# Kernel tuning notes

Hardware: AMD Instinct MI355X
Metric: run time of the kernel (lower is better)

The kernel has to match this reference:

```python
import jax, jax.numpy as jnp
import numpy as np

B, S, H = 2, 112, 768
M = 256     # cfg.mlp_hidden_size
L = 54      # vocab size of 'ent_rel_id' (joint labels)
O = 10      # ent_rel_file['q_num_logits']


def setup_inputs() -> dict:
    key = jax.random.key(0)
    ks = jax.random.split(key, 12)
    inp = {
        "seq_encoder_reprs": jax.random.normal(ks[0], (B, S, H), jnp.float32),
        "joint_label_matrix": jax.random.randint(ks[1], (B, S, S), 0, L),
        "joint_label_matrix_mask": jax.random.randint(ks[2], (B, S, S), 0, 2) > 0,
        "quintuplet_matrix": jax.random.randint(ks[3], (B, S, S, S), 0, O),
        "quintuplet_matrix_mask": jax.random.randint(ks[4], (B, S, S, S), 0, 2) > 0,
        # learned parameters (BertLinear = Linear + activation; dropout inactive at eval)
        "pair_w": jax.random.normal(ks[5], (2 * H, M), jnp.float32) * 0.02,
        "pair_b": jnp.zeros((M,), jnp.float32),
        "final_w": jax.random.normal(ks[6], (M, L), jnp.float32) * 0.02,
        "final_b": jnp.zeros((L,), jnp.float32),
        "value_w": jax.random.normal(ks[7], (H, M), jnp.float32) * 0.02,
        "value_b": jnp.zeros((M,), jnp.float32),
        # U is zero-initialized in the module; use small random values so the
        # triaffine path produces non-trivial numerics.
        "U": jax.random.normal(ks[8], (O, M, M), jnp.float32) * 0.02,
    }
    return inp


def _masked_ce(logits, labels, mask):
    # mean cross-entropy over masked positions (== CE over boolean-indexed rows)
    logp = jax.nn.log_softmax(logits, axis=-1)
    nll = -jnp.take_along_axis(logp, labels[..., None], axis=-1)[..., 0]
    m = mask.astype(logits.dtype)
    return jnp.sum(nll * m) / jnp.maximum(jnp.sum(m), 1.0)


def reference(seq_encoder_reprs, joint_label_matrix, joint_label_matrix_mask,
              quintuplet_matrix, quintuplet_matrix_mask,
              pair_w, pair_b, final_w, final_b, value_w, value_b, U):
    x = seq_encoder_reprs  # [B,S,H]
    # pair = cat(head_expand, tail_expand) -> pair_mlp (Linear + GELU)
    # split the Linear over the concat to avoid materializing [B,S,S,2H]:
    # cat([head,tail]) @ W == head @ W[:H] + tail @ W[H:]
    h_part = jnp.einsum('bxh,hm->bxm', x, pair_w[:H])   # head contribution
    t_part = jnp.einsum('byh,hm->bym', x, pair_w[H:])   # tail contribution
    pair = jax.nn.gelu(h_part[:, :, None, :] + t_part[:, None, :, :] + pair_b,
                       approximate=False)               # [B,S,S,M]
    joint_score = jnp.einsum('bxym,ml->bxyl', pair, final_w) + final_b  # [B,S,S,L]

    value = jax.nn.gelu(jnp.einsum('bzh,hm->bzm', x, value_w) + value_b,
                        approximate=False)              # [B,S,M]
    # triaffine: bxyi,oij,bzj->bxyzo ; contract value with U first (small interm.)
    vU = jnp.einsum('bzj,oij->bzoi', value, U)          # [B,S,O,M]
    q_score = jnp.einsum('bxyi,bzoi->bxyzo', pair, vU)  # [B,S,S,S,O]

    # q_loss: CrossEntropy applied to softmax(q_score) (as in the source)
    q_probs = jax.nn.softmax(q_score, axis=-1)
    q_loss = _masked_ce(q_probs, quintuplet_matrix, quintuplet_matrix_mask)
    element_loss = _masked_ce(joint_score, joint_label_matrix, joint_label_matrix_mask)
    loss = element_loss + q_loss
    return loss, joint_score, q_score
```

## Files before the change

### kernel.cpp

```cpp
#include <hip/hip_runtime.h>
#include <hip/hip_bf16.h>

#define BB 2
#define SS 112
#define HH 768
#define MM 256
#define LL 54
#define OO 10
#define NPAIR (BB*SS*SS)
#define NQPOS (BB*SS*SS*SS)
#define SO (SS*OO)
#define SOP 1152
#define S2 (SS*SS)
#define NQBLK (NQPOS/512)
#define NEBLK (NPAIR/256)

typedef short bf16x8 __attribute__((ext_vector_type(8)));
typedef float f32x4 __attribute__((ext_vector_type(4)));

#define WS_HP    64
#define WS_TP    57408
#define WS_VAL   114752
#define WS_UT    172096
#define WS_VUB   827456
#define WS_PAIRB 1122368
#define WS_FWB   4333632
#define WS_QPART 4341824
#define WS_EPART 4352800

__device__ __forceinline__ float gelu_exact(float v) {
    return 0.5f * v * (1.0f + erff(v * 0.70710678118654752f));
}

__global__ __launch_bounds__(256) void k_proj(const float* __restrict__ x,
                                              const float* __restrict__ pw,
                                              const float* __restrict__ vw,
                                              const float* __restrict__ vb,
                                              float* __restrict__ hp,
                                              float* __restrict__ tp,
                                              float* __restrict__ val) {
    __shared__ float xs[HH];
    const int row = blockIdx.x;
    const int sel = blockIdx.y;
    const float* xr = x + (long)row * HH;
    for (int i = threadIdx.x; i < HH; i += 256) xs[i] = xr[i];
    __syncthreads();
    const int m = threadIdx.x;
    const float* w = (sel == 0) ? pw : (sel == 1) ? (pw + (long)HH * MM) : vw;
    float a = 0.f;
    for (int h = 0; h < HH; ++h)
        a = fmaf(xs[h], w[(long)h * MM + m], a);
    if (sel == 0)      hp[(long)row * MM + m] = a;
    else if (sel == 1) tp[(long)row * MM + m] = a;
    else               val[(long)row * MM + m] = gelu_exact(a + vb[m]);
}

__global__ void k_transU(const float* __restrict__ U, float* __restrict__ UT) {
    __shared__ float t[32][33];
    const int o = blockIdx.z;
    const int i0 = blockIdx.x * 32, j0 = blockIdx.y * 32;
    const int tx = threadIdx.x, ty = threadIdx.y;
    for (int r = 0; r < 32; r += 8)
        t[ty + r][tx] = U[((long)(o * MM + i0 + ty + r)) * MM + j0 + tx];
    __syncthreads();
    for (int r = 0; r < 32; r += 8)
        UT[((long)(o * MM + j0 + ty + r)) * MM + i0 + tx] = t[tx][ty + r];
}

__global__ __launch_bounds__(256) void k_vU(const float* __restrict__ val,
                                            const float* __restrict__ UT,
                                            __hip_bfloat16* __restrict__ vub) {
    __shared__ float vs[8][MM];
    const int b = blockIdx.x / 14, zt = blockIdx.x % 14, o = blockIdx.y;
    const int z0 = zt * 8;
    for (int idx = threadIdx.x; idx < 8 * MM; idx += 256) {
        const int zz = idx >> 8, m = idx & 255;
        vs[zz][m] = val[((long)(b * SS + z0 + zz)) * MM + m];
    }
    __syncthreads();
    const int i = threadIdx.x;
    float acc[8];
#pragma unroll
    for (int zz = 0; zz < 8; ++zz) acc[zz] = 0.f;
    const float* utp = UT + (long)o * MM * MM + i;
    for (int j = 0; j < MM; ++j) {
        const float u = utp[(long)j * MM];
#pragma unroll
        for (int zz = 0; zz < 8; ++zz) acc[zz] = fmaf(vs[zz][j], u, acc[zz]);
    }
#pragma unroll
    for (int zz = 0; zz < 8; ++zz)
        vub[((long)b * SOP + (z0 + zz) * OO + o) * MM + i] = __float2bfloat16(acc[zz]);
}

__global__ __launch_bounds__(256) void k_prepB(const float* __restrict__ fw,
                                               __hip_bfloat16* __restrict__ fwb) {
    const int idx = blockIdx.x * 256 + threadIdx.x;
    const int c = idx >> 8, k = idx & 255;
    const float v = (c < LL) ? fw[(long)k * LL + c] : 0.f;
    fwb[idx] = __float2bfloat16(v);
}

__global__ __launch_bounds__(256) void k_pair(const float* __restrict__ hp,
                                              const float* __restrict__ tp,
                                              const float* __restrict__ pb,
                                              __hip_bfloat16* __restrict__ pairb) {
    __shared__ float hs[MM];
    const int bx = blockIdx.x;
    hs[threadIdx.x] = hp[(long)bx * MM + threadIdx.x] + pb[threadIdx.x];
    __syncthreads();
    const int b = bx / SS;
    const int half = threadIdx.x >> 7;
    const int m0 = (threadIdx.x & 127) * 2;
    const float h0 = hs[m0], h1 = hs[m0 + 1];
    const int y0base = blockIdx.y * 56;
    for (int y0 = y0base; y0 < y0base + 56; y0 += 2) {
        const int y = y0 + half;
        const float2 t2 = *(const float2*)(tp + ((long)(b * SS + y)) * MM + m0);
        __hip_bfloat162 o2;
        o2.x = __float2bfloat16(gelu_exact(h0 + t2.x));
        o2.y = __float2bfloat16(gelu_exact(h1 + t2.y));
        *(__hip_bfloat162*)(pairb + ((long)bx * SS + y) * MM + m0) = o2;
    }
}

__global__ __launch_bounds__(256) void k_jointg(const __hip_bfloat16* __restrict__ pairb,
                                                const __hip_bfloat16* __restrict__ fwb,
                                                const float* __restrict__ fb,
                                                float* __restrict__ joint) {
    __shared__ __align__(16) char Al[16384];
    __shared__ __align__(16) char Bl[8192];
    const int r0 = blockIdx.x * 128;
    const int tid = threadIdx.x;
    const int lane = tid & 63, wid = tid >> 6;
    const int rl = lane & 15, kb = lane >> 4;

    int arow[4], aci[4], wadA[4];
#pragma unroll
    for (int j = 0; j < 4; ++j) {
        const int chunk = tid + 256 * j;
        arow[j] = chunk >> 3; aci[j] = chunk & 7;
        wadA[j] = (arow[j] * 128 + aci[j] * 16) ^ ((arow[j] & 7) << 4);
    }
    int brow[2], bci[2], wadB[2];
#pragma unroll
    for (int j = 0; j < 2; ++j) {
        const int chunk = tid + 256 * j;
        brow[j] = chunk >> 3; bci[j] = chunk & 7;
        wadB[j] = (brow[j] * 128 + bci[j] * 16) ^ ((brow[j] & 7) << 4);
    }

    f32x4 acc[2][4] = {};
    float4 ra[4], rb[2];

    auto issue = [&](int kt) {
#pragma unroll
        for (int j = 0; j < 4; ++j)
            ra[j] = *(const float4*)((const char*)pairb +
                     ((long)(r0 + arow[j]) * MM + kt * 64 + aci[j] * 8) * 2);
#pragma unroll
        for (int j = 0; j < 2; ++j)
            rb[j] = *(const float4*)((const char*)fwb +
                     ((long)brow[j] * MM + kt * 64 + bci[j] * 8) * 2);
    };
    auto dowrite = [&]() {
#pragma unroll
        for (int j = 0; j < 4; ++j) *(float4*)(Al + wadA[j]) = ra[j];
#pragma unroll
        for (int j = 0; j < 2; ++j) *(float4*)(Bl + wadB[j]) = rb[j];
    };
    auto compute = [&]() {
#pragma unroll
        for (int ks = 0; ks < 2; ++ks) {
            bf16x8 af[2], bv[4];
#pragma unroll
            for (int m = 0; m < 2; ++m) {
                const int rr = wid * 32 + m * 16 + rl;
                af[m] = *(const bf16x8*)(Al + ((rr * 128 + ks * 64 + kb * 16) ^ ((rr & 7) << 4)));
            }
#pragma unroll
            for (int n = 0; n < 4; ++n) {
                const int cc = n * 16 + rl;
                bv[n] = *(const bf16x8*)(Bl + ((cc * 128 + ks * 64 + kb * 16) ^ ((cc & 7) << 4)));
            }
#pragma unroll
            for (int m = 0; m < 2; ++m)
#pragma unroll
                for (int n = 0; n < 4; ++n)
                    acc[m][n] = __builtin_amdgcn_mfma_f32_16x16x32_bf16(af[m], bv[n], acc[m][n], 0, 0, 0);
        }
    };

    issue(0); dowrite(); __syncthreads();
    for (int kt = 0; kt < 4; ++kt) {
        if (kt < 3) issue(kt + 1);
        compute();
        __syncthreads();
        if (kt < 3) { dowrite(); __syncthreads(); }
    }

#pragma unroll
    for (int m = 0; m < 2; ++m)
#pragma unroll
        for (int n = 0; n < 4; ++n) {
            const int col = n * 16 + rl;
            if (col < LL) {
                const float bias = fb[col];
                const int rbase = r0 + wid * 32 + m * 16 + kb * 4;
#pragma unroll
                for (int j = 0; j < 4; ++j)
                    joint[(long)(rbase + j) * LL + col] = acc[m][n][j] + bias;
            }
        }
}

__global__ __launch_bounds__(256) void k_qgemm(const __hip_bfloat16* __restrict__ pairb,
                                               const __hip_bfloat16* __restrict__ vub,
                                               float* __restrict__ qout) {
    __shared__ __align__(16) char Al[16384];
    __shared__ __align__(16) char Bl[16384];
    const int b = blockIdx.z;
    const int r0 = blockIdx.x * 128;
    const int c0 = blockIdx.y * 128;
    const __hip_bfloat16* A  = pairb + (long)b * S2 * MM;
    const __hip_bfloat16* Bm = vub + (long)b * SOP * MM;
    const int tid = threadIdx.x;
    const int lane = tid & 63, wid = tid >> 6;
    const int wr = wid >> 1, wc = wid & 1;
    const int rl = lane & 15, kb = lane >> 4;

    int arow[4], aci[4], wad[4];
#pragma unroll
    for (int j = 0; j < 4; ++j) {
        const int chunk = tid + 256 * j;
        arow[j] = chunk >> 3; aci[j] = chunk & 7;
        wad[j] = (arow[j] * 128 + aci[j] * 16) ^ ((arow[j] & 7) << 4);
    }

    f32x4 acc[4][4] = {};
    float4 ra[4], rb[4];

    auto issue = [&](int kt) {
#pragma unroll
        for (int j = 0; j < 4; ++j) {
            ra[j] = *(const float4*)((const char*)A +
                     ((long)(r0 + arow[j]) * MM + kt * 64 + aci[j] * 8) * 2);
            rb[j] = *(const float4*)((const char*)Bm +
                     ((long)(c0 + arow[j]) * MM + kt * 64 + aci[j] * 8) * 2);
        }
    };
    auto dowrite = [&]() {
#pragma unroll
        for (int j = 0; j < 4; ++j) {
            *(float4*)(Al + wad[j]) = ra[j];
            *(float4*)(Bl + wad[j]) = rb[j];
        }
    };
    auto compute = [&]() {
#pragma unroll
        for (int ks = 0; ks < 2; ++ks) {
            bf16x8 af[4], bv[4];
#pragma unroll
            for (int m = 0; m < 4; ++m) {
                const int rr = wr * 64 + m * 16 + rl;
                af[m] = *(const bf16x8*)(Al + ((rr * 128 + ks * 64 + kb * 16) ^ ((rr & 7) << 4)));
            }
#pragma unroll
            for (int n = 0; n < 4; ++n) {
                const int cc = wc * 64 + n * 16 + rl;
                bv[n] = *(const bf16x8*)(Bl + ((cc * 128 + ks * 64 + kb * 16) ^ ((cc & 7) << 4)));
            }
#pragma unroll
            for (int m = 0; m < 4; ++m)
#pragma unroll
                for (int n = 0; n < 4; ++n)
                    acc[m][n] = __builtin_amdgcn_mfma_f32_16x16x32_bf16(af[m], bv[n], acc[m][n], 0, 0, 0);
        }
    };

    issue(0); dowrite(); __syncthreads();
    for (int kt = 0; kt < 4; ++kt) {
        if (kt < 3) issue(kt + 1);
        compute();
        __syncthreads();
        if (kt < 3) { dowrite(); __syncthreads(); }
    }

    float* C = qout + (long)b * S2 * SO;
#pragma unroll
    for (int m = 0; m < 4; ++m)
#pragma unroll
        for (int n = 0; n < 4; ++n) {
            const int col = c0 + wc * 64 + n * 16 + rl;
            if (col < SO) {
                const int rbase = r0 + wr * 64 + m * 16 + kb * 4;
#pragma unroll
                for (int j = 0; j < 4; ++j)
                    C[(long)(rbase + j) * SO + col] = acc[m][n][j];
            }
        }
}

__device__ __forceinline__ void reduce2_part(float v1, float v2, float* slot) {
    const int lane = threadIdx.x & 63, wid = threadIdx.x >> 6;
#pragma unroll
    for (int off = 32; off > 0; off >>= 1) {
        v1 += __shfl_down(v1, off, 64);
        v2 += __shfl_down(v2, off, 64);
    }
    __shared__ float w1[4], w2[4];
    if (lane == 0) { w1[wid] = v1; w2[wid] = v2; }
    __syncthreads();
    if (threadIdx.x == 0) {
        slot[0] = w1[0] + w1[1] + w1[2] + w1[3];
        slot[1] = w2[0] + w2[1] + w2[2] + w2[3];
    }
}

__global__ __launch_bounds__(256) void k_elloss(const float* __restrict__ joint,
                                                const int* __restrict__ labels,
                                                const int* __restrict__ mask,
                                                float* __restrict__ epart) {
    __shared__ float js[256 * LL];
    const int base = blockIdx.x * 256;
    const float* src = joint + (long)base * LL;
    for (int i = threadIdx.x; i < 256 * LL; i += 256) js[i] = src[i];
    __syncthreads();
    const int idx = base + threadIdx.x;
    float nll = 0.f, cnt = 0.f;
    if (mask[idx] != 0) {
        const float* s = js + threadIdx.x * LL;
        float mx = -3.4e38f;
        for (int l = 0; l < LL; ++l) mx = fmaxf(mx, s[l]);
        float se = 0.f;
        for (int l = 0; l < LL; ++l) se += expf(s[l] - mx);
        nll = mx + logf(se) - s[labels[idx]];
        cnt = 1.f;
    }
    reduce2_part(nll, cnt, epart + 2 * blockIdx.x);
}

__global__ __launch_bounds__(256) void k_qloss(const float* __restrict__ q,
                                               const int* __restrict__ labels,
                                               const int* __restrict__ mask,
                                               float* __restrict__ qpart) {
    __shared__ float qs[512 * 11];
    const int base = blockIdx.x * 512;
    const float* src = q + (long)base * OO;
    for (int i = threadIdx.x; i < 512 * OO; i += 256) {
        const int p = i / 10, o = i - p * 10;
        qs[p * 11 + o] = src[i];
    }
    __syncthreads();
    float nll = 0.f, cnt = 0.f;
#pragma unroll
    for (int j = 0; j < 2; ++j) {
        const int p = threadIdx.x + 256 * j;
        const int gi = base + p;
        if (mask[gi] != 0) {
            const float* s = qs + p * 11;
            float r[OO];
#pragma unroll
            for (int o = 0; o < OO; ++o) r[o] = s[o];
            float mx = r[0];
#pragma unroll
            for (int o = 1; o < OO; ++o) mx = fmaxf(mx, r[o]);
            float se = 0.f;
#pragma unroll
            for (int o = 0; o < OO; ++o) { r[o] = expf(r[o] - mx); se += r[o]; }
            const float inv = 1.0f / se;
            float se2 = 0.f;
#pragma unroll
            for (int o = 0; o < OO; ++o) se2 += expf(r[o] * inv);
            const float plab = expf(s[labels[gi]] - mx) * inv;
            nll += logf(se2) - plab;
            cnt += 1.f;
        }
    }
    reduce2_part(nll, cnt, qpart + 2 * blockIdx.x);
}

__global__ __launch_bounds__(256) void k_final(const float* __restrict__ qpart,
                                               const float* __restrict__ epart,
                                               float* __restrict__ out) {
    __shared__ float s1[256], s2[256], s3[256], s4[256];
    float q1 = 0.f, q2 = 0.f, e1 = 0.f, e2 = 0.f;
    for (int i = threadIdx.x; i < NQBLK; i += 256) {
        q1 += qpart[2 * i]; q2 += qpart[2 * i + 1];
    }
    for (int i = threadIdx.x; i < NEBLK; i += 256) {
        e1 += epart[2 * i]; e2 += epart[2 * i + 1];
    }
    const int t = threadIdx.x;
    s1[t] = q1; s2[t] = q2; s3[t] = e1; s4[t] = e2;
    __syncthreads();
    for (int off = 128; off > 0; off >>= 1) {
        if (t < off) {
            s1[t] += s1[t + off]; s2[t] += s2[t + off];
            s3[t] += s3[t + off]; s4[t] += s4[t + off];
        }
        __syncthreads();
    }
    if (t == 0)
        out[0] = s3[0] / fmaxf(s4[0], 1.0f) + s1[0] / fmaxf(s2[0], 1.0f);
}

extern "C" void kernel_launch(void* const* d_in, const int* in_sizes, int n_in,
                              void* d_out, int out_size, void* d_ws, size_t ws_size,
                              hipStream_t stream) {
    const float* x     = (const float*)d_in[0];
    const int*   jlab  = (const int*)d_in[1];
    const int*   jmask = (const int*)d_in[2];
    const int*   qlab  = (const int*)d_in[3];
    const int*   qmask = (const int*)d_in[4];
    const float* pw    = (const float*)d_in[5];
    const float* pb    = (const float*)d_in[6];
    const float* fw    = (const float*)d_in[7];
    const float* fb    = (const float*)d_in[8];
    const float* vw    = (const float*)d_in[9];
    const float* vb    = (const float*)d_in[10];
    const float* U     = (const float*)d_in[11];

    float* out  = (float*)d_out;
    float* ws   = (float*)d_ws;
    float* hp   = ws + WS_HP;
    float* tp   = ws + WS_TP;
    float* val  = ws + WS_VAL;
    float* UT   = ws + WS_UT;
    __hip_bfloat16* vub   = (__hip_bfloat16*)(ws + WS_VUB);
    __hip_bfloat16* pairb = (__hip_bfloat16*)(ws + WS_PAIRB);
    __hip_bfloat16* fwb   = (__hip_bfloat16*)(ws + WS_FWB);
    float* qpart = ws + WS_QPART;
    float* epart = ws + WS_EPART;

    float* joint = out + 1;
    float* qsc   = out + 1 + (long)NPAIR * LL;

    k_proj<<<dim3(BB * SS, 3), 256, 0, stream>>>(x, pw, vw, vb, hp, tp, val);
    k_transU<<<dim3(8, 8, OO), dim3(32, 8), 0, stream>>>(U, UT);
    k_vU<<<dim3(BB * 14, OO), 256, 0, stream>>>(val, UT, vub);
    k_prepB<<<64, 256, 0, stream>>>(fw, fwb);
    k_pair<<<dim3(BB * SS, 2), 256, 0, stream>>>(hp, tp, pb, pairb);
    k_jointg<<<NPAIR / 128, 256, 0, stream>>>(pairb, fwb, fb, joint);
    k_qgemm<<<dim3(S2 / 128, 9, BB), 256, 0, stream>>>(pairb, vub, qsc);
    k_elloss<<<NEBLK, 256, 0, stream>>>(joint, jlab, jmask, epart);
    k_qloss<<<NQBLK, 256, 0, stream>>>(qsc, qlab, qmask, qpart);
    k_final<<<1, 256, 0, stream>>>(qpart, epart, out);
}
```

Measured before the change: 206.1 us.

## Merge prep kernels, fuse joint CE loss into GEMM epilogue, swap qgemm grid order

Merges the projection, U-transpose and final-weight conversion into one launch, and the vU and pair-GELU kernels into a second. The joint-score cross-entropy moves into the joint GEMM epilogue through a shared-memory staging tile, so the joint scores are no longer re-read from global memory and one launch disappears. The qgemm grid now runs column tiles fastest, so consecutive blocks share the same A rows, which may help L2 reuse. The price is larger shared memory in the joint GEMM and heterogeneous block roles within each merged kernel.

```diff
diff --git a/kernel.cpp b/kernel.cpp
--- a/kernel.cpp
+++ b/kernel.cpp
@@ -13,7 +13,7 @@
 #define SOP 1152
 #define S2 (SS*SS)
 #define NQBLK (NQPOS/512)
-#define NEBLK (NPAIR/256)
+#define NJBLK (NPAIR/128)
 
 typedef short bf16x8 __attribute__((ext_vector_type(8)));
 typedef float f32x4 __attribute__((ext_vector_type(4)));
@@ -32,104 +32,132 @@
     return 0.5f * v * (1.0f + erff(v * 0.70710678118654752f));
 }
 
-__global__ __launch_bounds__(256) void k_proj(const float* __restrict__ x,
-                                              const float* __restrict__ pw,
-                                              const float* __restrict__ vw,
-                                              const float* __restrict__ vb,
-                                              float* __restrict__ hp,
-                                              float* __restrict__ tp,
-                                              float* __restrict__ val) {
-    __shared__ float xs[HH];
-    const int row = blockIdx.x;
-    const int sel = blockIdx.y;
-    const float* xr = x + (long)row * HH;
-    for (int i = threadIdx.x; i < HH; i += 256) xs[i] = xr[i];
+__global__ __launch_bounds__(256) void k_pre(const float* __restrict__ x,
+                                             const float* __restrict__ pw,
+                                             const float* __restrict__ vw,
+                                             const float* __restrict__ vb,
+                                             const float* __restrict__ U,
+                                             const float* __restrict__ fw,
+                                             float* __restrict__ hp,
+                                             float* __restrict__ tp,
+                                             float* __restrict__ val,
+                                             float* __restrict__ UT,
+                                             __hip_bfloat16* __restrict__ fwb) {
+    __shared__ float sm[1056];
+    const int id = blockIdx.x;
+    const int tid = threadIdx.x;
+    if (id < 672) {
+        const int row = id % 224, sel = id / 224;
+        const float* xr = x + (long)row * HH;
+        for (int i = tid; i < HH; i += 256) sm[i] = xr[i];
+        __syncthreads();
+        const int m = tid;
+        const float* w = (sel == 0) ? pw : (sel == 1) ? (pw + (long)HH * MM) : vw;
+        float a = 0.f;
+        for (int h = 0; h < HH; ++h)
+            a = fmaf(sm[h], w[(long)h * MM + m], a);
+        if (sel == 0)      hp[(long)row * MM + m] = a;
+        else if (sel == 1) tp[(long)row * MM + m] = a;
+        else               val[(long)row * MM + m] = gelu_exact(a + vb[m]);
+    } else if (id < 1312) {
+        const int t = id - 672;
+        const int o = t / 64, rest = t % 64;
+        const int i0 = (rest >> 3) * 32, j0 = (rest & 7) * 32;
+        const int tx = tid & 31, ty = tid >> 5;
+        float (*tt)[33] = (float(*)[33])sm;
+        for (int r = 0; r < 32; r += 8)
+            tt[ty + r][tx] = U[((long)(o * MM + i0 + ty + r)) * MM + j0 + tx];
+        __syncthreads();
+        for (int r = 0; r < 32; r += 8)
+            UT[((long)(o * MM + j0 + ty + r)) * MM + i0 + tx] = tt[tx][ty + r];
+    } else {
+        const int idx2 = (id - 1312) * 256 + tid;
+        const int c = idx2 >> 8, k = idx2 & 255;
+        const float v = (c < LL) ? fw[(long)k * LL + c] : 0.f;
+        fwb[idx2] = __float2bfloat16(v);
+    }
+}
+
+__global__ __launch_bounds__(256) void k_mid(const float* __restrict__ val,
+                                             const float* __restrict__ UT,
+                                             __hip_bfloat16* __restrict__ vub,
+                                             const float* __restrict__ hp,
+                                             const float* __restrict__ tp,
+                                             const float* __restrict__ pb,
+                                             __hip_bfloat16* __restrict__ pairb) {
+    __shared__ float sm[8 * MM];
+    const int id = blockIdx.x;
+    const int tid = threadIdx.x;
+    if (id < 280) {
+        const int b = id / 140, r = id % 140;
+        const int o = r / 14, zt = r % 14;
+        const int z0 = zt * 8;
+        float (*vs)[MM] = (float(*)[MM])sm;
+        for (int idx = tid; idx < 8 * MM; idx += 256) {
+            const int zz = idx >> 8, m = idx & 255;
+            vs[zz][m] = val[((long)(b * SS + z0 + zz)) * MM + m];
+        }
+        __syncthreads();
+        const int i = tid;
+        float acc[8];
+#pragma unroll
+        for (int zz = 0; zz < 8; ++zz) acc[zz] = 0.f;
+        const float* utp = UT + (long)o * MM * MM + i;
+        for (int j = 0; j < MM; ++j) {
+            const float u = utp[(long)j * MM];
+#pragma unroll
+            for (int zz = 0; zz < 8; ++zz) acc[zz] = fmaf(vs[zz][j], u, acc[zz]);
+        }
+#pragma unroll
+        for (int zz = 0; zz < 8; ++zz)
+            vub[((long)b * SOP + (z0 + zz) * OO + o) * MM + i] = __float2bfloat16(acc[zz]);
+    } else {
+        const int p = id - 280;
+        const int bx = p % 224;
+        const int y0base = (p / 224) * 56;
+        sm[tid] = hp[(long)bx * MM + tid] + pb[tid];
+        __syncthreads();
+        const int b = bx / SS;
+        const int half = tid >> 7;
+        const int m0 = (tid & 127) * 2;
+        const float h0 = sm[m0], h1 = sm[m0 + 1];
+        for (int y0 = y0base; y0 < y0base + 56; y0 += 2) {
+            const int y = y0 + half;
+            const float2 t2 = *(const float2*)(tp + ((long)(b * SS + y)) * MM + m0);
+            __hip_bfloat162 o2;
+            o2.x = __float2bfloat16(gelu_exact(h0 + t2.x));
+            o2.y = __float2bfloat16(gelu_exact(h1 + t2.y));
+            *(__hip_bfloat162*)(pairb + ((long)bx * SS + y) * MM + m0) = o2;
+        }
+    }
+}
+
+__device__ __forceinline__ void reduce2_part(float v1, float v2, float* slot) {
+    const int lane = threadIdx.x & 63, wid = threadIdx.x >> 6;
+#pragma unroll
+    for (int off = 32; off > 0; off >>= 1) {
+        v1 += __shfl_down(v1, off, 64);
+        v2 += __shfl_down(v2, off, 64);
+    }
+    __shared__ float w1[4], w2[4];
+    if (lane == 0) { w1[wid] = v1; w2[wid] = v2; }
     __syncthreads();
-    const int m = threadIdx.x;
-    const float* w = (sel == 0) ? pw : (sel == 1) ? (pw + (long)HH * MM) : vw;
-    float a = 0.f;
-    for (int h = 0; h < HH; ++h)
-        a = fmaf(xs[h], w[(long)h * MM + m], a);
-    if (sel == 0)      hp[(long)row * MM + m] = a;
-    else if (sel == 1) tp[(long)row * MM + m] = a;
-    else               val[(long)row * MM + m] = gelu_exact(a + vb[m]);
-}
-
-__global__ void k_transU(const float* __restrict__ U, float* __restrict__ UT) {
-    __shared__ float t[32][33];
-    const int o = blockIdx.z;
-    const int i0 = blockIdx.x * 32, j0 = blockIdx.y * 32;
-    const int tx = threadIdx.x, ty = threadIdx.y;
-    for (int r = 0; r < 32; r += 8)
-        t[ty + r][tx] = U[((long)(o * MM + i0 + ty + r)) * MM + j0 + tx];
-    __syncthreads();
-    for (int r = 0; r < 32; r += 8)
-        UT[((long)(o * MM + j0 + ty + r)) * MM + i0 + tx] = t[tx][ty + r];
-}
-
-__global__ __launch_bounds__(256) void k_vU(const float* __restrict__ val,
-                                            const float* __restrict__ UT,
-                                            __hip_bfloat16* __restrict__ vub) {
-    __shared__ float vs[8][MM];
-    const int b = blockIdx.x / 14, zt = blockIdx.x % 14, o = blockIdx.y;
-    const int z0 = zt * 8;
-    for (int idx = threadIdx.x; idx < 8 * MM; idx += 256) {
-        const int zz = idx >> 8, m = idx & 255;
-        vs[zz][m] = val[((long)(b * SS + z0 + zz)) * MM + m];
-    }
-    __syncthreads();
-    const int i = threadIdx.x;
-    float acc[8];
-#pragma unroll
-    for (int zz = 0; zz < 8; ++zz) acc[zz] = 0.f;
-    const float* utp = UT + (long)o * MM * MM + i;
-    for (int j = 0; j < MM; ++j) {
-        const float u = utp[(long)j * MM];
-#pragma unroll
-        for (int zz = 0; zz < 8; ++zz) acc[zz] = fmaf(vs[zz][j], u, acc[zz]);
-    }
-#pragma unroll
-    for (int zz = 0; zz < 8; ++zz)
-        vub[((long)b * SOP + (z0 + zz) * OO + o) * MM + i] = __float2bfloat16(acc[zz]);
-}
-
-__global__ __launch_bounds__(256) void k_prepB(const float* __restrict__ fw,
-                                               __hip_bfloat16* __restrict__ fwb) {
-    const int idx = blockIdx.x * 256 + threadIdx.x;
-    const int c = idx >> 8, k = idx & 255;
-    const float v = (c < LL) ? fw[(long)k * LL + c] : 0.f;
-    fwb[idx] = __float2bfloat16(v);
-}
-
-__global__ __launch_bounds__(256) void k_pair(const float* __restrict__ hp,
-                                              const float* __restrict__ tp,
-                                              const float* __restrict__ pb,
-                                              __hip_bfloat16* __restrict__ pairb) {
-    __shared__ float hs[MM];
-    const int bx = blockIdx.x;
-    hs[threadIdx.x] = hp[(long)bx * MM + threadIdx.x] + pb[threadIdx.x];
-    __syncthreads();
-    const int b = bx / SS;
-    const int half = threadIdx.x >> 7;
-    const int m0 = (threadIdx.x & 127) * 2;
-    const float h0 = hs[m0], h1 = hs[m0 + 1];
-    const int y0base = blockIdx.y * 56;
-    for (int y0 = y0base; y0 < y0base + 56; y0 += 2) {
-        const int y = y0 + half;
-        const float2 t2 = *(const float2*)(tp + ((long)(b * SS + y)) * MM + m0);
-        __hip_bfloat162 o2;
-        o2.x = __float2bfloat16(gelu_exact(h0 + t2.x));
-        o2.y = __float2bfloat16(gelu_exact(h1 + t2.y));
-        *(__hip_bfloat162*)(pairb + ((long)bx * SS + y) * MM + m0) = o2;
+    if (threadIdx.x == 0) {
+        slot[0] = w1[0] + w1[1] + w1[2] + w1[3];
+        slot[1] = w2[0] + w2[1] + w2[2] + w2[3];
     }
 }
 
 __global__ __launch_bounds__(256) void k_jointg(const __hip_bfloat16* __restrict__ pairb,
                                                 const __hip_bfloat16* __restrict__ fwb,
                                                 const float* __restrict__ fb,
-                                                float* __restrict__ joint) {
-    __shared__ __align__(16) char Al[16384];
-    __shared__ __align__(16) char Bl[8192];
+                                                const int* __restrict__ jlab,
+                                                const int* __restrict__ jmask,
+                                                float* __restrict__ joint,
+                                                float* __restrict__ epart) {
+    __shared__ __align__(16) char smem[33280];
+    char* Al = smem;
+    char* Bl = smem + 16384;
     const int r0 = blockIdx.x * 128;
     const int tid = threadIdx.x;
     const int lane = tid & 63, wid = tid >> 6;
@@ -199,19 +227,39 @@
         if (kt < 3) { dowrite(); __syncthreads(); }
     }
 
+    float* stage = (float*)smem;
+    __syncthreads();
 #pragma unroll
     for (int m = 0; m < 2; ++m)
 #pragma unroll
         for (int n = 0; n < 4; ++n) {
             const int col = n * 16 + rl;
-            if (col < LL) {
-                const float bias = fb[col];
-                const int rbase = r0 + wid * 32 + m * 16 + kb * 4;
-#pragma unroll
-                for (int j = 0; j < 4; ++j)
-                    joint[(long)(rbase + j) * LL + col] = acc[m][n][j] + bias;
-            }
-        }
+            const float bias = (col < LL) ? fb[col] : 0.f;
+            const int lrow0 = wid * 32 + m * 16 + kb * 4;
+#pragma unroll
+            for (int j = 0; j < 4; ++j) {
+                const float v = acc[m][n][j] + bias;
+                if (col < LL)
+                    joint[(long)(r0 + lrow0 + j) * LL + col] = v;
+                stage[(lrow0 + j) * 65 + col] = v;
+            }
+        }
+    __syncthreads();
+
+    float nll = 0.f, cnt = 0.f;
+    if (tid < 128) {
+        const int gi = r0 + tid;
+        if (jmask[gi] != 0) {
+            const float* s = stage + tid * 65;
+            float mx = -3.4e38f;
+            for (int l = 0; l < LL; ++l) mx = fmaxf(mx, s[l]);
+            float se = 0.f;
+            for (int l = 0; l < LL; ++l) se += expf(s[l] - mx);
+            nll = mx + logf(se) - s[jlab[gi]];
+            cnt = 1.f;
+        }
+    }
+    reduce2_part(nll, cnt, epart + 2 * blockIdx.x);
 }
 
 __global__ __launch_bounds__(256) void k_qgemm(const __hip_bfloat16* __restrict__ pairb,
@@ -220,8 +268,8 @@
     __shared__ __align__(16) char Al[16384];
     __shared__ __align__(16) char Bl[16384];
     const int b = blockIdx.z;
-    const int r0 = blockIdx.x * 128;
-    const int c0 = blockIdx.y * 128;
+    const int r0 = blockIdx.y * 128;
+    const int c0 = blockIdx.x * 128;
     const __hip_bfloat16* A  = pairb + (long)b * S2 * MM;
     const __hip_bfloat16* Bm = vub + (long)b * SOP * MM;
     const int tid = threadIdx.x;
@@ -299,45 +347,6 @@
                     C[(long)(rbase + j) * SO + col] = acc[m][n][j];
             }
         }
-}
-
-__device__ __forceinline__ void reduce2_part(float v1, float v2, float* slot) {
-    const int lane = threadIdx.x & 63, wid = threadIdx.x >> 6;
-#pragma unroll
-    for (int off = 32; off > 0; off >>= 1) {
-        v1 += __shfl_down(v1, off, 64);
-        v2 += __shfl_down(v2, off, 64);
-    }
-    __shared__ float w1[4], w2[4];
-    if (lane == 0) { w1[wid] = v1; w2[wid] = v2; }
-    __syncthreads();
-    if (threadIdx.x == 0) {
-        slot[0] = w1[0] + w1[1] + w1[2] + w1[3];
-        slot[1] = w2[0] + w2[1] + w2[2] + w2[3];
-    }
-}
-
-__global__ __launch_bounds__(256) void k_elloss(const float* __restrict__ joint,
-                                                const int* __restrict__ labels,
-                                                const int* __restrict__ mask,
-                                                float* __restrict__ epart) {
-    __shared__ float js[256 * LL];
-    const int base = blockIdx.x * 256;
-    const float* src = joint + (long)base * LL;
-    for (int i = threadIdx.x; i < 256 * LL; i += 256) js[i] = src[i];
-    __syncthreads();
-    const int idx = base + threadIdx.x;
-    float nll = 0.f, cnt = 0.f;
-    if (mask[idx] != 0) {
-        const float* s = js + threadIdx.x * LL;
-        float mx = -3.4e38f;
-        for (int l = 0; l < LL; ++l) mx = fmaxf(mx, s[l]);
-        float se = 0.f;
-        for (int l = 0; l < LL; ++l) se += expf(s[l] - mx);
-        nll = mx + logf(se) - s[labels[idx]];
-        cnt = 1.f;
-    }
-    reduce2_part(nll, cnt, epart + 2 * blockIdx.x);
 }
 
 __global__ __launch_bounds__(256) void k_qloss(const float* __restrict__ q,
@@ -388,7 +397,7 @@
     for (int i = threadIdx.x; i < NQBLK; i += 256) {
         q1 += qpart[2 * i]; q2 += qpart[2 * i + 1];
     }
-    for (int i = threadIdx.x; i < NEBLK; i += 256) {
+    for (int i = threadIdx.x; i < NJBLK; i += 256) {
         e1 += epart[2 * i]; e2 += epart[2 * i + 1];
     }
     const int t = threadIdx.x;
@@ -436,14 +445,10 @@
     float* joint = out + 1;
     float* qsc   = out + 1 + (long)NPAIR * LL;
 
-    k_proj<<<dim3(BB * SS, 3), 256, 0, stream>>>(x, pw, vw, vb, hp, tp, val);
-    k_transU<<<dim3(8, 8, OO), dim3(32, 8), 0, stream>>>(U, UT);
-    k_vU<<<dim3(BB * 14, OO), 256, 0, stream>>>(val, UT, vub);
-    k_prepB<<<64, 256, 0, stream>>>(fw, fwb);
-    k_pair<<<dim3(BB * SS, 2), 256, 0, stream>>>(hp, tp, pb, pairb);
-    k_jointg<<<NPAIR / 128, 256, 0, stream>>>(pairb, fwb, fb, joint);
-    k_qgemm<<<dim3(S2 / 128, 9, BB), 256, 0, stream>>>(pairb, vub, qsc);
-    k_elloss<<<NEBLK, 256, 0, stream>>>(joint, jlab, jmask, epart);
+    k_pre<<<1376, 256, 0, stream>>>(x, pw, vw, vb, U, fw, hp, tp, val, UT, fwb);
+    k_mid<<<728, 256, 0, stream>>>(val, UT, vub, hp, tp, pb, pairb);
+    k_jointg<<<NJBLK, 256, 0, stream>>>(pairb, fwb, fb, jlab, jmask, joint, epart);
+    k_qgemm<<<dim3(9, 98, BB), 256, 0, stream>>>(pairb, vub, qsc);
     k_qloss<<<NQBLK, 256, 0, stream>>>(qsc, qlab, qmask, qpart);
     k_final<<<1, 256, 0, stream>>>(qpart, epart, out);
 }
```

Result: faster. 184.3 us (-10.6%).
